# Performance work log

Measured on AMD Instinct MI355X. Metric: run time of the kernel, lower is better.

The kernel has to match this reference:

```python
import jax, jax.numpy as jnp
import numpy as np

NUM_ACTS = 6  # relu, sigmoid, tanh, elu, leaky_relu(0.01), gelu

def _apply_all(xr):
    # xr: [B, N] -> [NUM_ACTS, B, N]
    return jnp.stack([
        jax.nn.relu(xr),
        jax.nn.sigmoid(xr),
        jnp.tanh(xr),
        jax.nn.elu(xr),
        jax.nn.leaky_relu(xr, negative_slope=0.01),
        jax.nn.gelu(xr),
    ], axis=0)

def setup_inputs() -> dict:
    key = jax.random.key(0)
    k1, k2 = jax.random.split(key)
    B, C, H, W = 64, 128, 56, 56
    x = jax.random.normal(k1, (B, C, H, W), dtype=jnp.float32)
    act_codes = jax.random.randint(k2, (C * H * W,), 0, NUM_ACTS, dtype=jnp.int32)
    return {"x": x, "act_codes": act_codes}

def reference(x, act_codes):
    B = x.shape[0]
    xr = x.reshape(B, -1)                      # [B, N], N = C*H*W
    stacked = _apply_all(xr)                   # [NUM_ACTS, B, N]
    idx = jnp.broadcast_to(act_codes[None, None, :].astype(jnp.int32),
                           (1,) + xr.shape)    # [1, B, N]
    out = jnp.take_along_axis(stacked, idx, axis=0)[0]  # per-column select
    return out.reshape(x.shape)
```

## Files before the change

### kernel.cpp

```cpp
#include <hip/hip_runtime.h>


#define N4 100352
#define GX 392
#define GY 64

typedef float f32x4 __attribute__((ext_vector_type(4)));

__device__ __forceinline__ float apply_act(float x, int c) {
    const float L2E = 1.4426950408889634f;

    bool c1 = (c == 1), c2 = (c == 2), c3 = (c == 3), c4 = (c == 4), c5 = (c == 5);
    bool pos = (x >= 0.f);

    float x2 = x * x;
    float tg = fmaf(0.0713548162f, x2, 1.5957691216f);
    float tm = c2 ? 2.f : (c5 ? tg : 1.f);
    float t  = x * tm;

    float e = __builtin_amdgcn_exp2f(-L2E * fabsf(t));
    float r = __builtin_amdgcn_rcpf(1.f + e);
    float s = pos ? r : e * r;

    float a = c5 ? x : (c2 ? 2.f : 1.f);
    float b = c2 ? -1.f : 0.f;
    float fam = fmaf(a, s, b);

    float neg  = c3 ? (e - 1.f) : (c4 ? 0.01f * x : 0.f);
    float triv = pos ? x : neg;

    bool isfam = c1 | c2 | c5;
    return isfam ? fam : triv;
}

__global__ __launch_bounds__(256) void act_select_kernel(
    const f32x4* __restrict__ x,
    const int4*  __restrict__ codes,
    f32x4*       __restrict__ out) {
    int n   = blockIdx.x * 256 + threadIdx.x;
    int idx = blockIdx.y * N4 + n;

    f32x4 v = x[idx];
    int4  c = codes[n];

    f32x4 o;
    o.x = apply_act(v.x, c.x);
    o.y = apply_act(v.y, c.y);
    o.z = apply_act(v.z, c.z);
    o.w = apply_act(v.w, c.w);

    __builtin_nontemporal_store(o, &out[idx]);
}

extern "C" void kernel_launch(void* const* d_in, const int* in_sizes, int n_in,
                              void* d_out, int out_size, void* d_ws, size_t ws_size,
                              hipStream_t stream) {
    const f32x4* x     = (const f32x4*)d_in[0];
    const int4*  codes = (const int4*)d_in[1];
    f32x4*       out   = (f32x4*)d_out;

    dim3 grid(GX, GY);
    act_select_kernel<<<grid, 256, 0, stream>>>(x, codes, out);
}
```

Before: 174.7 us.

## Process eight batch rows per thread and hoist per-column code decoding

Each thread now handles 8 batch rows for the same columns, so the activation codes are loaded and decoded into per-column constants once and reused across rows. The grid's y dimension shrinks from 64 to 8. The log2(e) scaling is folded into the precomputed constants to save a multiply per element. The nontemporal store is replaced by a plain store. This adds register pressure and lowers parallelism, and may change write-cache behavior, in exchange for less redundant code loading and select work in a memory-bound kernel.

```diff
diff --git a/kernel.cpp b/kernel.cpp
--- a/kernel.cpp
+++ b/kernel.cpp
@@ -1,55 +1,70 @@
 #include <hip/hip_runtime.h>
 
 
-#define N4 100352
-#define GX 392
-#define GY 64
+#define N4   100352
+#define GX   392
+#define ROWS 8
+#define GY   8
 
 typedef float f32x4 __attribute__((ext_vector_type(4)));
-
-__device__ __forceinline__ float apply_act(float x, int c) {
-    const float L2E = 1.4426950408889634f;
-
-    bool c1 = (c == 1), c2 = (c == 2), c3 = (c == 3), c4 = (c == 4), c5 = (c == 5);
-    bool pos = (x >= 0.f);
-
-    float x2 = x * x;
-    float tg = fmaf(0.0713548162f, x2, 1.5957691216f);
-    float tm = c2 ? 2.f : (c5 ? tg : 1.f);
-    float t  = x * tm;
-
-    float e = __builtin_amdgcn_exp2f(-L2E * fabsf(t));
-    float r = __builtin_amdgcn_rcpf(1.f + e);
-    float s = pos ? r : e * r;
-
-    float a = c5 ? x : (c2 ? 2.f : 1.f);
-    float b = c2 ? -1.f : 0.f;
-    float fam = fmaf(a, s, b);
-
-    float neg  = c3 ? (e - 1.f) : (c4 ? 0.01f * x : 0.f);
-    float triv = pos ? x : neg;
-
-    bool isfam = c1 | c2 | c5;
-    return isfam ? fam : triv;
-}
 
 __global__ __launch_bounds__(256) void act_select_kernel(
     const f32x4* __restrict__ x,
     const int4*  __restrict__ codes,
-    f32x4*       __restrict__ out) {
-    int n   = blockIdx.x * 256 + threadIdx.x;
-    int idx = blockIdx.y * N4 + n;
+    f32x4*       __restrict__ out)
+{
+    const float L2E = 1.4426950408889634f;
+    const float K0L = 1.5957691216f * L2E;
+    const float K1L = 0.0713548162f * L2E;
 
-    f32x4 v = x[idx];
-    int4  c = codes[n];
+    int n = blockIdx.x * 256 + threadIdx.x;
+    int4 c = codes[n];
+    int cc[4] = {c.x, c.y, c.z, c.w};
 
-    f32x4 o;
-    o.x = apply_act(v.x, c.x);
-    o.y = apply_act(v.y, c.y);
-    o.z = apply_act(v.z, c.z);
-    o.w = apply_act(v.w, c.w);
+    float tmL[4], aC[4], bC[4], ngC[4];
+    bool  c5b[4], c3b[4], famb[4];
+    #pragma unroll
+    for (int i = 0; i < 4; ++i) {
+        int ci = cc[i];
+        bool c1 = ci == 1, c2 = ci == 2;
+        c3b[i]  = ci == 3;
+        c5b[i]  = ci == 5;
+        famb[i] = c1 | c2 | c5b[i];
+        tmL[i]  = c2 ? 2.f * L2E : L2E;
+        aC[i]   = c2 ? 2.f : 1.f;
+        bC[i]   = c2 ? -1.f : 0.f;
+        ngC[i]  = (ci == 4) ? 0.01f : 0.f;
+    }
 
-    __builtin_nontemporal_store(o, &out[idx]);
+    const f32x4* xb = x   + (size_t)blockIdx.y * ROWS * N4 + n;
+    f32x4*       ob = out + (size_t)blockIdx.y * ROWS * N4 + n;
+
+    #pragma unroll
+    for (int r = 0; r < ROWS; ++r) {
+        f32x4 v = xb[(size_t)r * N4];
+        f32x4 o;
+        #pragma unroll
+        for (int i = 0; i < 4; ++i) {
+            float xv  = v[i];
+            float ax  = fabsf(xv);
+            bool  pos = xv >= 0.f;
+
+            float tgL = fmaf(K1L, xv * xv, K0L);
+            float tL  = c5b[i] ? tgL : tmL[i];
+            float e   = __builtin_amdgcn_exp2f(-tL * ax);
+            float rc  = __builtin_amdgcn_rcpf(1.f + e);
+            float s   = pos ? rc : e * rc;
+
+            float a   = c5b[i] ? xv : aC[i];
+            float fam = fmaf(a, s, bC[i]);
+
+            float neg = c3b[i] ? (e - 1.f) : ngC[i] * xv;
+            float tr  = pos ? xv : neg;
+
+            o[i] = famb[i] ? fam : tr;
+        }
+        ob[(size_t)r * N4] = o;
+    }
 }
 
 extern "C" void kernel_launch(void* const* d_in, const int* in_sizes, int n_in,
```

New measurement: 182.1 us. 1.04x slower.
